# Kernel optimization log

Measured on AMD Instinct MI355X. Metric: run time of the kernel, lower is better.

## Reference

```python
import jax, jax.numpy as jnp
import numpy as np

B = 64        # batch
N = 10000     # num_nodes
D = 66        # input_dim + hid_dim
O = 64        # output_dim
K = 2         # max_diffusion_step
E = 160000    # edges per support


def _spmm(rows, cols, vals, x):
    # sparse (N,N) @ dense (N,F) via scatter-add: y[r] += v * x[c]
    return jnp.zeros_like(x).at[rows].add(vals[:, None] * x[cols])


def setup_inputs() -> dict:
    key = jax.random.key(0)
    ks = jax.random.split(key, 10)
    inputs = jax.random.normal(ks[0], (B, N * D), dtype=jnp.float32)
    state = jax.random.normal(ks[1], (B, N * 64), dtype=jnp.float32)  # unused by forward
    weight = jax.random.normal(ks[2], (D * (2 * K + 1), O), dtype=jnp.float32) * 0.05
    biases = jnp.zeros((O,), dtype=jnp.float32)
    rows0 = jax.random.randint(ks[3], (E,), 0, N, dtype=jnp.int32)
    cols0 = jax.random.randint(ks[4], (E,), 0, N, dtype=jnp.int32)
    vals0 = jax.random.uniform(ks[5], (E,), dtype=jnp.float32) / 16.0
    rows1 = jax.random.randint(ks[6], (E,), 0, N, dtype=jnp.int32)
    cols1 = jax.random.randint(ks[7], (E,), 0, N, dtype=jnp.int32)
    vals1 = jax.random.uniform(ks[8], (E,), dtype=jnp.float32) / 16.0
    return {"inputs": inputs, "state": state, "weight": weight, "biases": biases,
            "vals0": vals0, "vals1": vals1, "rows0": rows0, "cols0": cols0,
            "rows1": rows1, "cols1": cols1}


def reference(inputs, state, weight, biases, vals0, vals1, rows0, cols0, rows1, cols1):
    del state  # accepted but unused, as in the original module
    x = inputs.reshape(B, N, D)
    x0 = jnp.transpose(x, (1, 2, 0)).reshape(N, D * B)  # [N, D*B]
    xs = [x0]
    for rows, cols, vals in ((rows0, cols0, vals0), (rows1, cols1, vals1)):
        x1 = _spmm(rows, cols, vals, x0)
        xs.append(x1)
        xk_1, xk_2 = x1, x0
        for _ in range(2, K + 1):
            x2 = 2.0 * _spmm(rows, cols, vals, xk_1) - xk_2  # Chebyshev recursion
            xs.append(x2)
            xk_1, xk_2 = x2, xk_1
    M = len(xs)  # num_matrices = 2*K + 1
    xcat = jnp.stack(xs, axis=0)                       # [M, N, D*B]
    xcat = xcat.reshape(M, N, D, B)
    xcat = jnp.transpose(xcat, (3, 1, 2, 0))            # [B, N, D, M]
    xcat = xcat.reshape(B * N, D * M)
    out = xcat @ weight + biases                        # [B*N, O]
    return out.reshape(B, N * O)
```

## Files before the change

### kernel.cpp

```cpp
#include <hip/hip_runtime.h>

#define NN 10000
#define NE 160000
#define ROWU 2112
#define OUTSTRIDE 640000

typedef unsigned int uint;
typedef unsigned short ushort;
typedef __attribute__((ext_vector_type(8))) short short8;
typedef __attribute__((ext_vector_type(4))) float f32x4;

__device__ __forceinline__ float bflo(uint u) { return __uint_as_float(u << 16); }
__device__ __forceinline__ float bfhi(uint u) { return __uint_as_float(u & 0xffff0000u); }
__device__ __forceinline__ uint packbf(float a, float b) {
    uint ua = __float_as_uint(a); ua += 0x7fffu + ((ua >> 16) & 1u);
    uint ub = __float_as_uint(b); ub += 0x7fffu + ((ub >> 16) & 1u);
    return (ua >> 16) | (ub & 0xffff0000u);
}

__global__ __launch_bounds__(256) void transpose_kernel(const float* __restrict__ in,
                                                        uint* __restrict__ x0) {
    const int n = blockIdx.x, t = threadIdx.x;
    const float* src = in + (size_t)n * 66;
    uint* dst = x0 + (size_t)n * ROWU;
#pragma unroll
    for (int j = 0; j < 9; j++) {
        const int ui = 256 * j + t;
        if (ui < ROWU) {
            const int idx = 2 * ui;
            const int b = (int)(((long long)idx * 63551) >> 22);
            const int d = idx - 66 * b;
            const float a0 = src[(size_t)b * 660000 + d];
            const float a1 = src[(size_t)b * 660000 + d + 1];
            dst[ui] = packbf(a0, a1);
        }
    }
}

__global__ void hist_kernel(const int* __restrict__ rows, int* __restrict__ cnt) {
    const int e = blockIdx.x * 256 + threadIdx.x;
    atomicAdd(&cnt[rows[e]], 1);
}

__global__ __launch_bounds__(1024) void scan_kernel(const int* __restrict__ cnt,
                                                    int* __restrict__ rp,
                                                    int* __restrict__ cur) {
    __shared__ int sums[1024];
    const int t = threadIdx.x;
    const int base = t * 10;
    int vals[10];
    int local = 0;
#pragma unroll
    for (int i = 0; i < 10; i++) {
        const int idx = base + i;
        const int v = (idx < NN) ? cnt[idx] : 0;
        vals[i] = local;
        local += v;
    }
    sums[t] = local;
    __syncthreads();
    for (int off = 1; off < 1024; off <<= 1) {
        const int v = (t >= off) ? sums[t - off] : 0;
        __syncthreads();
        sums[t] += v;
        __syncthreads();
    }
    const int excl = (t == 0) ? 0 : sums[t - 1];
#pragma unroll
    for (int i = 0; i < 10; i++) {
        const int idx = base + i;
        if (idx < NN) {
            const int v = excl + vals[i];
            rp[idx] = v;
            cur[idx] = v;
        }
    }
    if (t == 1023) rp[NN] = sums[1023];
}

__global__ void scatter_kernel(const int* __restrict__ rows, const int* __restrict__ cols,
                               const float* __restrict__ vals, int* __restrict__ cur,
                               int* __restrict__ scols, float* __restrict__ svals) {
    const int e = blockIdx.x * 256 + threadIdx.x;
    const int r = rows[e];
    const int p = atomicAdd(&cur[r], 1);
    scols[p] = cols[e];
    svals[p] = vals[e];
}

__global__ __launch_bounds__(256) void wprep_kernel(const float* __restrict__ weight,
                                                    ushort* __restrict__ Wt) {
    const int t = threadIdx.x;
    const int o = t & 63, rep = t >> 6;
    for (int kk = 0; kk < 88; kk++) {
        const int k = rep * 88 + kk;
        float v = 0.f;
        if (k < 330) {
            const int m = (int)(((long long)k * 63551) >> 22);
            const int d = k - 66 * m;
            v = weight[(d * 5 + m) * 64 + o];
        }
        uint uv = __float_as_uint(v);
        uv += 0x7fffu + ((uv >> 16) & 1u);
        Wt[o * 352 + k] = (ushort)(uv >> 16);
    }
}

__global__ __launch_bounds__(256) void spmm_kernel(const int* __restrict__ rp,
                                                   const int* __restrict__ scols,
                                                   const float* __restrict__ svals,
                                                   const uint* __restrict__ x,
                                                   const uint* __restrict__ z,
                                                   uint* __restrict__ y, float alpha) {
    const int n = blockIdx.x, t = threadIdx.x;
    float acc[18];
#pragma unroll
    for (int i = 0; i < 18; i++) acc[i] = 0.f;
    const int e0 = rp[n], e1 = rp[n + 1];
    for (int e = e0; e < e1; e++) {
        const int c = scols[e];
        const float v = alpha * svals[e];
        const uint* src = x + (size_t)c * ROWU;
#pragma unroll
        for (int k = 0; k < 8; k++) {
            const uint u = src[t + 256 * k];
            acc[2 * k]     = fmaf(v, bflo(u), acc[2 * k]);
            acc[2 * k + 1] = fmaf(v, bfhi(u), acc[2 * k + 1]);
        }
        if (t < 64) {
            const uint u = src[2048 + t];
            acc[16] = fmaf(v, bflo(u), acc[16]);
            acc[17] = fmaf(v, bfhi(u), acc[17]);
        }
    }
    uint* yr = y + (size_t)n * ROWU;
    if (z) {
        const uint* zr = z + (size_t)n * ROWU;
#pragma unroll
        for (int k = 0; k < 8; k++) {
            const uint uz = zr[t + 256 * k];
            yr[t + 256 * k] = packbf(acc[2 * k] - bflo(uz), acc[2 * k + 1] - bfhi(uz));
        }
        if (t < 64) {
            const uint uz = zr[2048 + t];
            yr[2048 + t] = packbf(acc[16] - bflo(uz), acc[17] - bfhi(uz));
        }
    } else {
#pragma unroll
        for (int k = 0; k < 8; k++)
            yr[t + 256 * k] = packbf(acc[2 * k], acc[2 * k + 1]);
        if (t < 64)
            yr[2048 + t] = packbf(acc[16], acc[17]);
    }
}

__global__ __launch_bounds__(256) void gemm_kernel(const uint* __restrict__ p0,
                                                   const uint* __restrict__ p1,
                                                   const uint* __restrict__ p2,
                                                   const uint* __restrict__ p3,
                                                   const uint* __restrict__ p4,
                                                   const ushort* __restrict__ Wt,
                                                   const float* __restrict__ bias,
                                                   float* __restrict__ out) {
    __shared__ ushort Xt[64 * 360];
    const int n = blockIdx.x, t = threadIdx.x;

#pragma unroll
    for (int m = 0; m < 5; m++) {
        const uint* src = (m == 0) ? p0 : (m == 1) ? p1 : (m == 2) ? p2 : (m == 3) ? p3 : p4;
        src += (size_t)n * ROWU;
#pragma unroll
        for (int j = 0; j < 9; j++) {
            const int flat = 256 * j + t;
            if (flat < ROWU) {
                const int b = (int)(((long long)flat * 127101) >> 22);
                const int i = flat - 33 * b;
                *(uint*)&Xt[b * 360 + m * 66 + 2 * i] = src[b * 33 + i];
            }
        }
    }
    if (t < 64) {
#pragma unroll
        for (int i = 0; i < 15; i++)
            *(uint*)&Xt[t * 360 + 330 + 2 * i] = 0u;
    }
    __syncthreads();

    const int w = t >> 6;
    const int l = t & 63;
    const int q = l >> 4;
    const int r = l & 15;

    short8 afr[11];
#pragma unroll
    for (int s = 0; s < 11; s++)
        afr[s] = *(const short8*)&Wt[(16 * w + r) * 352 + s * 32 + q * 8];

    const float4 bv = *(const float4*)&bias[16 * w + 4 * q];

#pragma unroll
    for (int bt = 0; bt < 4; bt++) {
        f32x4 acc = {0.f, 0.f, 0.f, 0.f};
        const ushort* xrow = &Xt[(16 * bt + r) * 360];
#pragma unroll
        for (int s = 0; s < 11; s++) {
            const short8 bfr = *(const short8*)&xrow[s * 32 + q * 8];
            acc = __builtin_amdgcn_mfma_f32_16x16x32_bf16(afr[s], bfr, acc, 0, 0, 0);
        }
        float4 res;
        res.x = acc[0] + bv.x;
        res.y = acc[1] + bv.y;
        res.z = acc[2] + bv.z;
        res.w = acc[3] + bv.w;
        *(float4*)&out[(size_t)(16 * bt + r) * OUTSTRIDE + (size_t)n * 64 + 16 * w + 4 * q] = res;
    }
}

extern "C" void kernel_launch(void* const* d_in, const int* in_sizes, int n_in,
                              void* d_out, int out_size, void* d_ws, size_t ws_size,
                              hipStream_t stream) {
    const float* inputs = (const float*)d_in[0];
    const float* weight = (const float*)d_in[2];
    const float* biases = (const float*)d_in[3];
    const float* vals0  = (const float*)d_in[4];
    const float* vals1  = (const float*)d_in[5];
    const int*   rows0  = (const int*)d_in[6];
    const int*   cols0  = (const int*)d_in[7];
    const int*   rows1  = (const int*)d_in[8];
    const int*   cols1  = (const int*)d_in[9];
    float* out = (float*)d_out;

    const size_t SZX = (size_t)NN * ROWU;
    uint* x0  = (uint*)d_ws;
    uint* xa0 = x0 + SZX;
    uint* xb0 = xa0 + SZX;
    uint* xa1 = xb0 + SZX;
    uint* xb1 = xa1 + SZX;
    ushort* Wt = (ushort*)(xb1 + SZX);
    int* cnt0 = (int*)(Wt + 64 * 352);
    int* cnt1 = cnt0 + NN;
    int* rp0  = cnt1 + NN;
    int* rp1  = rp0 + (NN + 1);
    int* cur0 = rp1 + (NN + 1);
    int* cur1 = cur0 + NN;
    int* sc0  = cur1 + NN;
    int* sc1  = sc0 + NE;
    float* sv0 = (float*)(sc1 + NE);
    float* sv1 = sv0 + NE;

    hipMemsetAsync(cnt0, 0, 2 * NN * sizeof(int), stream);
    transpose_kernel<<<NN, 256, 0, stream>>>(inputs, x0);

    hist_kernel<<<NE / 256, 256, 0, stream>>>(rows0, cnt0);
    hist_kernel<<<NE / 256, 256, 0, stream>>>(rows1, cnt1);
    scan_kernel<<<1, 1024, 0, stream>>>(cnt0, rp0, cur0);
    scan_kernel<<<1, 1024, 0, stream>>>(cnt1, rp1, cur1);
    scatter_kernel<<<NE / 256, 256, 0, stream>>>(rows0, cols0, vals0, cur0, sc0, sv0);
    scatter_kernel<<<NE / 256, 256, 0, stream>>>(rows1, cols1, vals1, cur1, sc1, sv1);
    wprep_kernel<<<1, 256, 0, stream>>>(weight, Wt);

    spmm_kernel<<<NN, 256, 0, stream>>>(rp0, sc0, sv0, x0, nullptr, xa0, 1.f);
    spmm_kernel<<<NN, 256, 0, stream>>>(rp0, sc0, sv0, xa0, x0, xb0, 2.f);
    spmm_kernel<<<NN, 256, 0, stream>>>(rp1, sc1, sv1, x0, nullptr, xa1, 1.f);
    spmm_kernel<<<NN, 256, 0, stream>>>(rp1, sc1, sv1, xa1, x0, xb1, 2.f);

    gemm_kernel<<<NN, 256, 0, stream>>>(x0, xa0, xb0, xa1, xb1, Wt, biases, out);
}
```

Baseline: 1.513 ms.

## Fold Chebyshev terms into weights, batch supports per launch, vectorize SpMM

The Chebyshev recursion 2*A*x1 - x0 is moved into the weight matrix: the x0 weight becomes W0-W2-W4, and W2 and W4 are doubled, so the second SpMM becomes a plain A*x1 with no z read or alpha. Both supports are merged into single launches for the hist, scan, scatter and SpMM kernels. The SpMM now uses uint4 loads and processes two edges per iteration. The GEMM is split into two blocks per node, each handling 32 batch rows. The weight folding changes bf16 rounding, which risks small accuracy drift.

```diff
diff --git a/kernel.cpp b/kernel.cpp
--- a/kernel.cpp
+++ b/kernel.cpp
@@ -37,14 +37,26 @@
     }
 }
 
-__global__ void hist_kernel(const int* __restrict__ rows, int* __restrict__ cnt) {
-    const int e = blockIdx.x * 256 + threadIdx.x;
+__global__ __launch_bounds__(256) void hist_kernel(const int* __restrict__ r0,
+                                                   const int* __restrict__ r1,
+                                                   int* __restrict__ c0,
+                                                   int* __restrict__ c1) {
+    const int bid = blockIdx.x;
+    const bool sB = bid >= (NE / 256);
+    const int e = (sB ? bid - NE / 256 : bid) * 256 + threadIdx.x;
+    const int* rows = sB ? r1 : r0;
+    int* cnt = sB ? c1 : c0;
     atomicAdd(&cnt[rows[e]], 1);
 }
 
-__global__ __launch_bounds__(1024) void scan_kernel(const int* __restrict__ cnt,
-                                                    int* __restrict__ rp,
-                                                    int* __restrict__ cur) {
+__global__ __launch_bounds__(1024) void scan_kernel(const int* __restrict__ c0,
+                                                    int* __restrict__ rp0_, int* __restrict__ cur0_,
+                                                    const int* __restrict__ c1,
+                                                    int* __restrict__ rp1_, int* __restrict__ cur1_) {
+    const int s = blockIdx.x;
+    const int* cnt = s ? c1 : c0;
+    int* rp  = s ? rp1_  : rp0_;
+    int* cur = s ? cur1_ : cur0_;
     __shared__ int sums[1024];
     const int t = threadIdx.x;
     const int base = t * 10;
@@ -78,10 +90,21 @@
     if (t == 1023) rp[NN] = sums[1023];
 }
 
-__global__ void scatter_kernel(const int* __restrict__ rows, const int* __restrict__ cols,
-                               const float* __restrict__ vals, int* __restrict__ cur,
-                               int* __restrict__ scols, float* __restrict__ svals) {
-    const int e = blockIdx.x * 256 + threadIdx.x;
+__global__ __launch_bounds__(256) void scatter_kernel(
+        const int* __restrict__ r0, const int* __restrict__ c0, const float* __restrict__ v0,
+        const int* __restrict__ r1, const int* __restrict__ c1, const float* __restrict__ v1,
+        int* __restrict__ cur0, int* __restrict__ cur1,
+        int* __restrict__ sc0_, float* __restrict__ sv0_,
+        int* __restrict__ sc1_, float* __restrict__ sv1_) {
+    const int bid = blockIdx.x;
+    const bool sB = bid >= (NE / 256);
+    const int e = (sB ? bid - NE / 256 : bid) * 256 + threadIdx.x;
+    const int* rows = sB ? r1 : r0;
+    const int* cols = sB ? c1 : c0;
+    const float* vals = sB ? v1 : v0;
+    int* cur = sB ? cur1 : cur0;
+    int* scols = sB ? sc1_ : sc0_;
+    float* svals = sB ? sv1_ : sv0_;
     const int r = rows[e];
     const int p = atomicAdd(&cur[r], 1);
     scols[p] = cols[e];
@@ -98,7 +121,15 @@
         if (k < 330) {
             const int m = (int)(((long long)k * 63551) >> 22);
             const int d = k - 66 * m;
-            v = weight[(d * 5 + m) * 64 + o];
+            if (m == 0)
+                v = weight[(d * 5 + 0) * 64 + o] - weight[(d * 5 + 2) * 64 + o]
+                    - weight[(d * 5 + 4) * 64 + o];
+            else if (m == 2)
+                v = 2.f * weight[(d * 5 + 2) * 64 + o];
+            else if (m == 4)
+                v = 2.f * weight[(d * 5 + 4) * 64 + o];
+            else
+                v = weight[(d * 5 + m) * 64 + o];
         }
         uint uv = __float_as_uint(v);
         uv += 0x7fffu + ((uv >> 16) & 1u);
@@ -106,52 +137,72 @@
     }
 }
 
-__global__ __launch_bounds__(256) void spmm_kernel(const int* __restrict__ rp,
-                                                   const int* __restrict__ scols,
-                                                   const float* __restrict__ svals,
-                                                   const uint* __restrict__ x,
-                                                   const uint* __restrict__ z,
-                                                   uint* __restrict__ y, float alpha) {
-    const int n = blockIdx.x, t = threadIdx.x;
-    float acc[18];
-#pragma unroll
-    for (int i = 0; i < 18; i++) acc[i] = 0.f;
+__device__ __forceinline__ void acc8(float* a, float v, uint4 u) {
+    a[0] = fmaf(v, bflo(u.x), a[0]); a[1] = fmaf(v, bfhi(u.x), a[1]);
+    a[2] = fmaf(v, bflo(u.y), a[2]); a[3] = fmaf(v, bfhi(u.y), a[3]);
+    a[4] = fmaf(v, bflo(u.z), a[4]); a[5] = fmaf(v, bfhi(u.z), a[5]);
+    a[6] = fmaf(v, bflo(u.w), a[6]); a[7] = fmaf(v, bfhi(u.w), a[7]);
+}
+__device__ __forceinline__ uint4 pack8(const float* a) {
+    uint4 r;
+    r.x = packbf(a[0], a[1]); r.y = packbf(a[2], a[3]);
+    r.z = packbf(a[4], a[5]); r.w = packbf(a[6], a[7]);
+    return r;
+}
+
+__global__ __launch_bounds__(256) void spmm_kernel(
+        const int* __restrict__ rpA, const int* __restrict__ scA, const float* __restrict__ svA,
+        const uint* __restrict__ xA, uint* __restrict__ yA,
+        const int* __restrict__ rpB, const int* __restrict__ scB, const float* __restrict__ svB,
+        const uint* __restrict__ xB, uint* __restrict__ yB) {
+    const int bid = blockIdx.x;
+    const bool sB = bid >= NN;
+    const int n = sB ? bid - NN : bid;
+    const int* __restrict__ rp = sB ? rpB : rpA;
+    const int* __restrict__ sc = sB ? scB : scA;
+    const float* __restrict__ sv = sB ? svB : svA;
+    const uint* __restrict__ x = sB ? xB : xA;
+    uint* __restrict__ y = sB ? yB : yA;
+    const int t = threadIdx.x;
+
+    float acc[24];
+#pragma unroll
+    for (int i = 0; i < 24; i++) acc[i] = 0.f;
+
     const int e0 = rp[n], e1 = rp[n + 1];
-    for (int e = e0; e < e1; e++) {
-        const int c = scols[e];
-        const float v = alpha * svals[e];
-        const uint* src = x + (size_t)c * ROWU;
-#pragma unroll
-        for (int k = 0; k < 8; k++) {
-            const uint u = src[t + 256 * k];
-            acc[2 * k]     = fmaf(v, bflo(u), acc[2 * k]);
-            acc[2 * k + 1] = fmaf(v, bfhi(u), acc[2 * k + 1]);
-        }
-        if (t < 64) {
-            const uint u = src[2048 + t];
-            acc[16] = fmaf(v, bflo(u), acc[16]);
-            acc[17] = fmaf(v, bfhi(u), acc[17]);
-        }
-    }
-    uint* yr = y + (size_t)n * ROWU;
-    if (z) {
-        const uint* zr = z + (size_t)n * ROWU;
-#pragma unroll
-        for (int k = 0; k < 8; k++) {
-            const uint uz = zr[t + 256 * k];
-            yr[t + 256 * k] = packbf(acc[2 * k] - bflo(uz), acc[2 * k + 1] - bfhi(uz));
-        }
-        if (t < 64) {
-            const uint uz = zr[2048 + t];
-            yr[2048 + t] = packbf(acc[16] - bflo(uz), acc[17] - bfhi(uz));
-        }
-    } else {
-#pragma unroll
-        for (int k = 0; k < 8; k++)
-            yr[t + 256 * k] = packbf(acc[2 * k], acc[2 * k + 1]);
-        if (t < 64)
-            yr[2048 + t] = packbf(acc[16], acc[17]);
-    }
+    int e = e0;
+    for (; e + 2 <= e1; e += 2) {
+        const int cA = sc[e], cB = sc[e + 1];
+        const float vA = sv[e], vB = sv[e + 1];
+        const uint4* ra = (const uint4*)(x + (size_t)cA * ROWU);
+        const uint4* rb = (const uint4*)(x + (size_t)cB * ROWU);
+        const uint4 a0 = ra[t], a1 = ra[t + 256];
+        const uint4 b0 = rb[t], b1 = rb[t + 256];
+        acc8(acc + 0, vA, a0); acc8(acc + 8, vA, a1);
+        acc8(acc + 0, vB, b0); acc8(acc + 8, vB, b1);
+        if (t < 16) {
+            const uint4 a2 = ra[512 + t];
+            const uint4 b2 = rb[512 + t];
+            acc8(acc + 16, vA, a2);
+            acc8(acc + 16, vB, b2);
+        }
+    }
+    if (e < e1) {
+        const int cA = sc[e];
+        const float vA = sv[e];
+        const uint4* ra = (const uint4*)(x + (size_t)cA * ROWU);
+        const uint4 a0 = ra[t], a1 = ra[t + 256];
+        acc8(acc + 0, vA, a0); acc8(acc + 8, vA, a1);
+        if (t < 16) {
+            const uint4 a2 = ra[512 + t];
+            acc8(acc + 16, vA, a2);
+        }
+    }
+
+    uint4* yr = (uint4*)(y + (size_t)n * ROWU);
+    yr[t] = pack8(acc + 0);
+    yr[t + 256] = pack8(acc + 8);
+    if (t < 16) yr[512 + t] = pack8(acc + 16);
 }
 
 __global__ __launch_bounds__(256) void gemm_kernel(const uint* __restrict__ p0,
@@ -162,24 +213,26 @@
                                                    const ushort* __restrict__ Wt,
                                                    const float* __restrict__ bias,
                                                    float* __restrict__ out) {
-    __shared__ ushort Xt[64 * 360];
-    const int n = blockIdx.x, t = threadIdx.x;
+    __shared__ ushort Xt[32 * 360];
+    const int bid = blockIdx.x;
+    const int n = bid >> 1, half = bid & 1;
+    const int t = threadIdx.x;
 
 #pragma unroll
     for (int m = 0; m < 5; m++) {
         const uint* src = (m == 0) ? p0 : (m == 1) ? p1 : (m == 2) ? p2 : (m == 3) ? p3 : p4;
-        src += (size_t)n * ROWU;
-#pragma unroll
-        for (int j = 0; j < 9; j++) {
+        src += (size_t)n * ROWU + half * 1056;
+#pragma unroll
+        for (int j = 0; j < 5; j++) {
             const int flat = 256 * j + t;
-            if (flat < ROWU) {
+            if (flat < 1056) {
                 const int b = (int)(((long long)flat * 127101) >> 22);
                 const int i = flat - 33 * b;
-                *(uint*)&Xt[b * 360 + m * 66 + 2 * i] = src[b * 33 + i];
+                *(uint*)&Xt[b * 360 + m * 66 + 2 * i] = src[flat];
             }
         }
     }
-    if (t < 64) {
+    if (t < 32) {
 #pragma unroll
         for (int i = 0; i < 15; i++)
             *(uint*)&Xt[t * 360 + 330 + 2 * i] = 0u;
@@ -199,7 +252,7 @@
     const float4 bv = *(const float4*)&bias[16 * w + 4 * q];
 
 #pragma unroll
-    for (int bt = 0; bt < 4; bt++) {
+    for (int bt = 0; bt < 2; bt++) {
         f32x4 acc = {0.f, 0.f, 0.f, 0.f};
         const ushort* xrow = &Xt[(16 * bt + r) * 360];
 #pragma unroll
@@ -212,7 +265,8 @@
         res.y = acc[1] + bv.y;
         res.z = acc[2] + bv.z;
         res.w = acc[3] + bv.w;
-        *(float4*)&out[(size_t)(16 * bt + r) * OUTSTRIDE + (size_t)n * 64 + 16 * w + 4 * q] = res;
+        const int bglob = 32 * half + 16 * bt + r;
+        *(float4*)&out[(size_t)bglob * OUTSTRIDE + (size_t)n * 64 + 16 * w + 4 * q] = res;
     }
 }
 
@@ -251,18 +305,17 @@
     hipMemsetAsync(cnt0, 0, 2 * NN * sizeof(int), stream);
     transpose_kernel<<<NN, 256, 0, stream>>>(inputs, x0);
 
-    hist_kernel<<<NE / 256, 256, 0, stream>>>(rows0, cnt0);
-    hist_kernel<<<NE / 256, 256, 0, stream>>>(rows1, cnt1);
-    scan_kernel<<<1, 1024, 0, stream>>>(cnt0, rp0, cur0);
-    scan_kernel<<<1, 1024, 0, stream>>>(cnt1, rp1, cur1);
-    scatter_kernel<<<NE / 256, 256, 0, stream>>>(rows0, cols0, vals0, cur0, sc0, sv0);
-    scatter_kernel<<<NE / 256, 256, 0, stream>>>(rows1, cols1, vals1, cur1, sc1, sv1);
+    hist_kernel<<<2 * (NE / 256), 256, 0, stream>>>(rows0, rows1, cnt0, cnt1);
+    scan_kernel<<<2, 1024, 0, stream>>>(cnt0, rp0, cur0, cnt1, rp1, cur1);
+    scatter_kernel<<<2 * (NE / 256), 256, 0, stream>>>(rows0, cols0, vals0,
+                                                       rows1, cols1, vals1,
+                                                       cur0, cur1, sc0, sv0, sc1, sv1);
     wprep_kernel<<<1, 256, 0, stream>>>(weight, Wt);
 
-    spmm_kernel<<<NN, 256, 0, stream>>>(rp0, sc0, sv0, x0, nullptr, xa0, 1.f);
-    spmm_kernel<<<NN, 256, 0, stream>>>(rp0, sc0, sv0, xa0, x0, xb0, 2.f);
-    spmm_kernel<<<NN, 256, 0, stream>>>(rp1, sc1, sv1, x0, nullptr, xa1, 1.f);
-    spmm_kernel<<<NN, 256, 0, stream>>>(rp1, sc1, sv1, xa1, x0, xb1, 2.f);
-
-    gemm_kernel<<<NN, 256, 0, stream>>>(x0, xa0, xb0, xa1, xb1, Wt, biases, out);
-}
+    spmm_kernel<<<2 * NN, 256, 0, stream>>>(rp0, sc0, sv0, x0, xa0,
+                                            rp1, sc1, sv1, x0, xa1);
+    spmm_kernel<<<2 * NN, 256, 0, stream>>>(rp0, sc0, sv0, xa0, xb0,
+                                            rp1, sc1, sv1, xa1, xb1);
+
+    gemm_kernel<<<2 * NN, 256, 0, stream>>>(x0, xa0, xb0, xa1, xb1, Wt, biases, out);
+}
```

New measurement: 1.448 ms. -4.3%, faster.
